# Kernel optimization log

Measured on AMD Instinct MI355X. Metric: run time of the kernel, lower is better.

## Reference

```python
import jax, jax.numpy as jnp
import numpy as np

TOP_P = 0.9
NEG_FILL = -1000000000.0


def _top_p_mask(logits):
    # probabilities over vocab
    probs = jax.nn.softmax(logits, axis=-1)
    # sort descending; keep the permutation to scatter the mask back
    order = jnp.argsort(-probs, axis=-1)                      # [B, V]
    ordered = jnp.take_along_axis(probs, order, axis=-1)      # [B, V]
    cum = jnp.cumsum(ordered, axis=-1)
    cum = cum.at[..., -1].set(0.0)
    cum = jnp.roll(cum, shift=1, axis=-1)                     # exclusive cumsum
    cmask = cum <= TOP_P                                      # [B, V] in sorted order
    # scatter back: selection[b, order[b, j]] = cmask[b, j]  <=>  gather by inverse perm
    inv = jnp.argsort(order, axis=-1)
    return jnp.take_along_axis(cmask, inv, axis=-1)


def setup_inputs() -> dict:
    key = jax.random.key(0)
    k1, k2 = jax.random.split(key)
    B, V = 256, 128000
    logits = jax.random.normal(k1, (B, V), dtype=jnp.float32)
    u = jax.random.uniform(k2, (B,), dtype=jnp.float32)
    return {"logits": logits, "u": u, "temperature": 1}


def reference(logits, u, temperature):
    t = jnp.asarray(temperature, dtype=logits.dtype)
    logits = logits / t
    sel = _top_p_mask(logits)
    masked = jnp.where(sel, logits, jnp.asarray(NEG_FILL, logits.dtype))
    probs = jax.nn.softmax(masked, axis=-1)                   # [B, V]
    # multinomial(num_samples=1) via inverse-CDF with uniform u
    cdf = jnp.cumsum(probs, axis=-1)
    token = jnp.sum(cdf < u[:, None], axis=-1)
    return jnp.minimum(token, probs.shape[-1] - 1)
```

## Files before the change

### kernel.cpp

```cpp
#include <hip/hip_runtime.h>

#define BLOCK 1024
#define NW (BLOCK / 64)
#define FPSCALE 8192.0f
#define INVSCALE 0x1p-13f

__device__ __forceinline__ float wincl(float v, int lane) {
#pragma unroll
    for (int o = 1; o < 64; o <<= 1) {
        float x = __shfl_up(v, o, 64);
        if (lane >= o) v += x;
    }
    return v;
}

__device__ __forceinline__ void find_crit_desc(const float* h, int n, int seg,
                                               float limit, int lane, int* out_b) {
    float segsum = 0.f;
    int start = n - 1 - lane * seg;
    for (int k = 0; k < seg; k++) segsum += h[start - k];
    float incl = wincl(segsum, lane);
    unsigned long long mk = __ballot(incl > limit);
    if (mk == 0ULL) { *out_b = 0; return; }
    int fl = __ffsll(mk) - 1;
    float base = __shfl(incl, fl, 64) - __shfl(segsum, fl, 64);
    int sstart = n - 1 - fl * seg;
    float v = (lane < seg) ? h[sstart - lane] : 0.f;
    float incl2 = wincl(v, lane);
    unsigned long long mk2 = __ballot((lane < seg) && (base + incl2 > limit));
    int k2 = mk2 ? (__ffsll(mk2) - 1) : (seg - 1);
    *out_b = sstart - k2;
}

#define OKEY(bb) ((bb) ^ ((unsigned)((int)(bb) >> 31) | 0x80000000u))

#define LD4(j) (*(const float4*)(row + (j)))

__global__ __launch_bounds__(BLOCK) void NucleusSampling_79336635892529_kernel(
    const float* __restrict__ logits, const float* __restrict__ uvec,
    const int* __restrict__ temp, int* __restrict__ out, int Vv) {
    const int b = blockIdx.x;
    const float* __restrict__ row = logits + (size_t)b * (size_t)Vv;
    const int t = threadIdx.x;
    const int lane = t & 63;
    const int wave = t >> 6;
    const int rep = lane & 3;

    __shared__ __align__(16) unsigned histbuf[8192];
    __shared__ float mg[2048];
    __shared__ float sweep[NW];
    __shared__ float csum[128];
    __shared__ int shb1;

    const float inv_t = 1.0f / (float)temp[0];
    const int V4 = Vv & ~3;
    const int S = BLOCK * 4;
    const int nch = (Vv + 1023) >> 10;

    for (int i = t; i < 8192; i += BLOCK) histbuf[i] = 0u;
    __syncthreads();

#define P1(xx) { unsigned kk = OKEY(__float_as_uint(xx)); \
                 float e = __expf((xx) * inv_t); \
                 atomicAdd(&histbuf[((kk >> 21) << 2) | rep], \
                           (unsigned)(e * FPSCALE + 0.5f)); }
    {
        int i = t * 4;
        bool have = (i + 3 * S + 3 < V4);
        float4 a0, a1, a2, a3;
        if (have) { a0 = LD4(i); a1 = LD4(i + S); a2 = LD4(i + 2 * S); a3 = LD4(i + 3 * S); }
        while (have) {
            const int ni = i + 4 * S;
            const bool nhave = (ni + 3 * S + 3 < V4);
            float4 n0, n1, n2, n3;
            if (nhave) { n0 = LD4(ni); n1 = LD4(ni + S); n2 = LD4(ni + 2 * S); n3 = LD4(ni + 3 * S); }
            P1(a0.x); P1(a0.y); P1(a0.z); P1(a0.w);
            P1(a1.x); P1(a1.y); P1(a1.z); P1(a1.w);
            P1(a2.x); P1(a2.y); P1(a2.z); P1(a2.w);
            P1(a3.x); P1(a3.y); P1(a3.z); P1(a3.w);
            a0 = n0; a1 = n1; a2 = n2; a3 = n3;
            i = ni; have = nhave;
        }
        for (; i < V4; i += S) { float4 a = LD4(i); P1(a.x); P1(a.y); P1(a.z); P1(a.w); }
        for (int j = V4 + t; j < Vv; j += BLOCK) P1(row[j]);
    }
    __syncthreads();

    float zp = 0.f;
    for (int i = t; i < 2048; i += BLOCK) {
        uint4 m4 = *(const uint4*)&histbuf[i << 2];
        float m = (float)(m4.x + m4.y + m4.z + m4.w) * INVSCALE;
        mg[i] = m;
        zp += m;
    }
#pragma unroll
    for (int o = 32; o >= 1; o >>= 1) zp += __shfl_xor(zp, o, 64);
    if (lane == 0) sweep[wave] = zp;
    __syncthreads();
    float Z = 0.f;
    for (int w = 0; w < NW; w++) Z += sweep[w];
    const float limit = 0.9f * Z;

    if (wave == 0) {
        int b1w;
        find_crit_desc(mg, 2048, 32, limit, lane, &b1w);
        if (lane == 0) shb1 = b1w;
    }
    if (t < 128 && t >= nch) csum[t] = 0.f;
    __syncthreads();
    const unsigned Tlow = (unsigned)shb1 << 21;

#define P2(xx, ss) { unsigned kk = OKEY(__float_as_uint(xx)); \
                     float e = __expf((xx) * inv_t); \
                     if (kk >= Tlow) ss += e; }
    for (int c0 = wave; c0 < nch; c0 += 4 * NW) {
        int cc0 = c0, cc1 = c0 + NW, cc2 = c0 + 2 * NW, cc3 = c0 + 3 * NW;
        float4 buf[4][4];
        bool val[4], full[4];
        int cbase[4] = {cc0 << 10, cc1 << 10, cc2 << 10, cc3 << 10};
        int cidx[4] = {cc0, cc1, cc2, cc3};
#pragma unroll
        for (int q = 0; q < 4; q++) {
            val[q] = (cidx[q] < nch);
            full[q] = val[q] && (cbase[q] + 1024 <= Vv);
            if (full[q]) {
                buf[q][0] = LD4(cbase[q] + lane * 4);
                buf[q][1] = LD4(cbase[q] + 256 + lane * 4);
                buf[q][2] = LD4(cbase[q] + 512 + lane * 4);
                buf[q][3] = LD4(cbase[q] + 768 + lane * 4);
            }
        }
#pragma unroll
        for (int q = 0; q < 4; q++) {
            if (!val[q]) continue;
            float s = 0.f;
            if (full[q]) {
#pragma unroll
                for (int r = 0; r < 4; r++) {
                    P2(buf[q][r].x, s); P2(buf[q][r].y, s);
                    P2(buf[q][r].z, s); P2(buf[q][r].w, s);
                }
            } else {
                for (int qq = 0; qq < 16; qq++) {
                    int i = cbase[q] + (qq << 6) + lane;
                    if (i < Vv) { float x = row[i]; P2(x, s); }
                }
            }
#pragma unroll
            for (int o = 32; o >= 1; o >>= 1) s += __shfl_xor(s, o, 64);
            if (lane == 0) csum[cidx[q]] = s;
        }
    }
    __syncthreads();

    if (wave == 0) {
        float segsum = csum[lane * 2] + csum[lane * 2 + 1];
        float incl = wincl(segsum, lane);
        float total = __shfl(incl, 63, 64);
        const float U = uvec[b] * total;
        unsigned long long mk = __ballot(incl >= U);
        int token;
        if (mk == 0ULL) {
            token = Vv;
        } else {
            int fl = __ffsll(mk) - 1;
            float base = __shfl(incl, fl, 64) - __shfl(segsum, fl, 64);
            float v = (lane < 2) ? csum[fl * 2 + lane] : 0.f;
            float incl2 = wincl(v, lane);
            unsigned long long mk2 = __ballot((lane < 2) && (base + incl2 >= U));
            int k2i = mk2 ? (__ffsll(mk2) - 1) : 1;
            int cx = fl * 2 + k2i;
            float B = base + __shfl(incl2, k2i, 64) - __shfl(v, k2i, 64);
            int cb = cx << 10;
            float vv[16];
#pragma unroll
            for (int r = 0; r < 16; r++) {
                int idx = cb + r * 64 + lane;
                vv[r] = (idx < Vv) ? row[idx] : -1e30f;
            }
            int cnt2 = 0;
#pragma unroll
            for (int r = 0; r < 16; r++) {
                int idx = cb + r * 64 + lane;
                unsigned kk = OKEY(__float_as_uint(vv[r]));
                float e = __expf(vv[r] * inv_t);
                float keep = (kk >= Tlow) ? e : 0.f;
                float is = wincl(keep, lane);
                unsigned long long mm = __ballot((idx < Vv) && (B + is < U));
                cnt2 += __popcll(mm);
                B += __shfl(is, 63, 64);
            }
            token = cb + cnt2;
        }
        if (lane == 0) out[b] = (token < Vv - 1) ? token : (Vv - 1);
    }
}

extern "C" void kernel_launch(void* const* d_in, const int* in_sizes, int n_in,
                              void* d_out, int out_size, void* d_ws, size_t ws_size,
                              hipStream_t stream) {
    const float* logits = (const float*)d_in[0];
    const float* u = (const float*)d_in[1];
    const int* temp = (const int*)d_in[2];
    int* out = (int*)d_out;
    int B = in_sizes[1];
    int V = in_sizes[0] / B;
    NucleusSampling_79336635892529_kernel<<<B, BLOCK, 0, stream>>>(logits, u, temp, out, V);
}
```

Measured before the change: 210.9 us.

## Keep half of each wave's row slice in registers between histogram and sum passes

Each wave now owns a contiguous block of eight 1024-element chunks. The first four chunks are loaded into registers and kept across the threshold-finding step, so the second pass reuses them instead of reloading from global or L2 memory. The remaining four chunks are still reloaded in pairs. This cuts second-pass memory traffic roughly in half at the cost of 64 extra live VGPRs per thread with 1024-thread blocks. It also assumes each wave covers 8192 elements, which only spans the whole row when V is at most 131072.

```diff
diff --git a/kernel.cpp b/kernel.cpp
--- a/kernel.cpp
+++ b/kernel.cpp
@@ -36,6 +36,15 @@
 
 #define LD4(j) (*(const float4*)(row + (j)))
 
+#define P1(xx) { unsigned kk = OKEY(__float_as_uint(xx)); \
+                 float e = __expf((xx) * inv_t); \
+                 atomicAdd(&histbuf[((kk >> 21) << 2) | rep], \
+                           (unsigned)(e * FPSCALE + 0.5f)); }
+
+#define P2(xx, ss) { unsigned kk = OKEY(__float_as_uint(xx)); \
+                     float e = __expf((xx) * inv_t); \
+                     if (kk >= Tlow) ss += e; }
+
 __global__ __launch_bounds__(BLOCK) void NucleusSampling_79336635892529_kernel(
     const float* __restrict__ logits, const float* __restrict__ uvec,
     const int* __restrict__ temp, int* __restrict__ out, int Vv) {
@@ -53,36 +62,70 @@
     __shared__ int shb1;
 
     const float inv_t = 1.0f / (float)temp[0];
-    const int V4 = Vv & ~3;
-    const int S = BLOCK * 4;
     const int nch = (Vv + 1023) >> 10;
 
     for (int i = t; i < 8192; i += BLOCK) histbuf[i] = 0u;
-    __syncthreads();
-
-#define P1(xx) { unsigned kk = OKEY(__float_as_uint(xx)); \
-                 float e = __expf((xx) * inv_t); \
-                 atomicAdd(&histbuf[((kk >> 21) << 2) | rep], \
-                           (unsigned)(e * FPSCALE + 0.5f)); }
-    {
-        int i = t * 4;
-        bool have = (i + 3 * S + 3 < V4);
-        float4 a0, a1, a2, a3;
-        if (have) { a0 = LD4(i); a1 = LD4(i + S); a2 = LD4(i + 2 * S); a3 = LD4(i + 3 * S); }
-        while (have) {
-            const int ni = i + 4 * S;
-            const bool nhave = (ni + 3 * S + 3 < V4);
-            float4 n0, n1, n2, n3;
-            if (nhave) { n0 = LD4(ni); n1 = LD4(ni + S); n2 = LD4(ni + 2 * S); n3 = LD4(ni + 3 * S); }
-            P1(a0.x); P1(a0.y); P1(a0.z); P1(a0.w);
-            P1(a1.x); P1(a1.y); P1(a1.z); P1(a1.w);
-            P1(a2.x); P1(a2.y); P1(a2.z); P1(a2.w);
-            P1(a3.x); P1(a3.y); P1(a3.z); P1(a3.w);
-            a0 = n0; a1 = n1; a2 = n2; a3 = n3;
-            i = ni; have = nhave;
-        }
-        for (; i < V4; i += S) { float4 a = LD4(i); P1(a.x); P1(a.y); P1(a.z); P1(a.w); }
-        for (int j = V4 + t; j < Vv; j += BLOCK) P1(row[j]);
+    if (t < 128) csum[t] = 0.f;
+    __syncthreads();
+
+    const int base0 = wave << 13;
+    float4 r[4][4];
+
+#pragma unroll
+    for (int c = 0; c < 4; c++) {
+        const int bA = base0 + (c << 10);
+        if (bA + 1024 <= Vv) {
+#pragma unroll
+            for (int q = 0; q < 4; q++) r[c][q] = LD4(bA + (q << 8) + (lane << 2));
+        }
+    }
+#pragma unroll
+    for (int c = 0; c < 4; c++) {
+        const int bA = base0 + (c << 10);
+        if (bA + 1024 <= Vv) {
+#pragma unroll
+            for (int q = 0; q < 4; q++) {
+                P1(r[c][q].x); P1(r[c][q].y); P1(r[c][q].z); P1(r[c][q].w);
+            }
+        } else if (bA < Vv) {
+            for (int qq = 0; qq < 16; qq++) {
+                int i = bA + (qq << 6) + lane;
+                if (i < Vv) P1(row[i]);
+            }
+        }
+    }
+#pragma unroll
+    for (int p = 0; p < 2; p++) {
+        const int bA = base0 + ((4 + 2 * p) << 10);
+        const int bB = bA + 1024;
+        const bool fa = (bA + 1024 <= Vv), fb = (bB + 1024 <= Vv);
+        float4 ta[4], tb[4];
+        if (fa) {
+#pragma unroll
+            for (int q = 0; q < 4; q++) ta[q] = LD4(bA + (q << 8) + (lane << 2));
+        }
+        if (fb) {
+#pragma unroll
+            for (int q = 0; q < 4; q++) tb[q] = LD4(bB + (q << 8) + (lane << 2));
+        }
+        if (fa) {
+#pragma unroll
+            for (int q = 0; q < 4; q++) { P1(ta[q].x); P1(ta[q].y); P1(ta[q].z); P1(ta[q].w); }
+        } else if (bA < Vv) {
+            for (int qq = 0; qq < 16; qq++) {
+                int i = bA + (qq << 6) + lane;
+                if (i < Vv) P1(row[i]);
+            }
+        }
+        if (fb) {
+#pragma unroll
+            for (int q = 0; q < 4; q++) { P1(tb[q].x); P1(tb[q].y); P1(tb[q].z); P1(tb[q].w); }
+        } else if (bB < Vv) {
+            for (int qq = 0; qq < 16; qq++) {
+                int i = bB + (qq << 6) + lane;
+                if (i < Vv) P1(row[i]);
+            }
+        }
     }
     __syncthreads();
 
@@ -106,49 +149,86 @@
         find_crit_desc(mg, 2048, 32, limit, lane, &b1w);
         if (lane == 0) shb1 = b1w;
     }
-    if (t < 128 && t >= nch) csum[t] = 0.f;
     __syncthreads();
     const unsigned Tlow = (unsigned)shb1 << 21;
 
-#define P2(xx, ss) { unsigned kk = OKEY(__float_as_uint(xx)); \
-                     float e = __expf((xx) * inv_t); \
-                     if (kk >= Tlow) ss += e; }
-    for (int c0 = wave; c0 < nch; c0 += 4 * NW) {
-        int cc0 = c0, cc1 = c0 + NW, cc2 = c0 + 2 * NW, cc3 = c0 + 3 * NW;
-        float4 buf[4][4];
-        bool val[4], full[4];
-        int cbase[4] = {cc0 << 10, cc1 << 10, cc2 << 10, cc3 << 10};
-        int cidx[4] = {cc0, cc1, cc2, cc3};
-#pragma unroll
-        for (int q = 0; q < 4; q++) {
-            val[q] = (cidx[q] < nch);
-            full[q] = val[q] && (cbase[q] + 1024 <= Vv);
-            if (full[q]) {
-                buf[q][0] = LD4(cbase[q] + lane * 4);
-                buf[q][1] = LD4(cbase[q] + 256 + lane * 4);
-                buf[q][2] = LD4(cbase[q] + 512 + lane * 4);
-                buf[q][3] = LD4(cbase[q] + 768 + lane * 4);
-            }
-        }
-#pragma unroll
-        for (int q = 0; q < 4; q++) {
-            if (!val[q]) continue;
-            float s = 0.f;
-            if (full[q]) {
-#pragma unroll
-                for (int r = 0; r < 4; r++) {
-                    P2(buf[q][r].x, s); P2(buf[q][r].y, s);
-                    P2(buf[q][r].z, s); P2(buf[q][r].w, s);
-                }
-            } else {
-                for (int qq = 0; qq < 16; qq++) {
-                    int i = cbase[q] + (qq << 6) + lane;
-                    if (i < Vv) { float x = row[i]; P2(x, s); }
-                }
-            }
-#pragma unroll
-            for (int o = 32; o >= 1; o >>= 1) s += __shfl_xor(s, o, 64);
-            if (lane == 0) csum[cidx[q]] = s;
+#pragma unroll
+    for (int c = 0; c < 4; c++) {
+        const int cc = (wave << 3) + c;
+        const int bA = base0 + (c << 10);
+        if (bA + 1024 <= Vv) {
+            float s = 0.f;
+#pragma unroll
+            for (int q = 0; q < 4; q++) {
+                P2(r[c][q].x, s); P2(r[c][q].y, s); P2(r[c][q].z, s); P2(r[c][q].w, s);
+            }
+#pragma unroll
+            for (int o = 32; o >= 1; o >>= 1) s += __shfl_xor(s, o, 64);
+            if (lane == 0) csum[cc] = s;
+        } else if (bA < Vv) {
+            float s = 0.f;
+            for (int qq = 0; qq < 16; qq++) {
+                int i = bA + (qq << 6) + lane;
+                if (i < Vv) { float x = row[i]; P2(x, s); }
+            }
+#pragma unroll
+            for (int o = 32; o >= 1; o >>= 1) s += __shfl_xor(s, o, 64);
+            if (lane == 0) csum[cc] = s;
+        }
+    }
+#pragma unroll
+    for (int p = 0; p < 2; p++) {
+        const int ccA = (wave << 3) + 4 + 2 * p;
+        const int ccB = ccA + 1;
+        const int bA = base0 + ((4 + 2 * p) << 10);
+        const int bB = bA + 1024;
+        const bool fa = (bA + 1024 <= Vv), fb = (bB + 1024 <= Vv);
+        float4 ta[4], tb[4];
+        if (fa) {
+#pragma unroll
+            for (int q = 0; q < 4; q++) ta[q] = LD4(bA + (q << 8) + (lane << 2));
+        }
+        if (fb) {
+#pragma unroll
+            for (int q = 0; q < 4; q++) tb[q] = LD4(bB + (q << 8) + (lane << 2));
+        }
+        if (fa) {
+            float s = 0.f;
+#pragma unroll
+            for (int q = 0; q < 4; q++) {
+                P2(ta[q].x, s); P2(ta[q].y, s); P2(ta[q].z, s); P2(ta[q].w, s);
+            }
+#pragma unroll
+            for (int o = 32; o >= 1; o >>= 1) s += __shfl_xor(s, o, 64);
+            if (lane == 0) csum[ccA] = s;
+        } else if (bA < Vv) {
+            float s = 0.f;
+            for (int qq = 0; qq < 16; qq++) {
+                int i = bA + (qq << 6) + lane;
+                if (i < Vv) { float x = row[i]; P2(x, s); }
+            }
+#pragma unroll
+            for (int o = 32; o >= 1; o >>= 1) s += __shfl_xor(s, o, 64);
+            if (lane == 0) csum[ccA] = s;
+        }
+        if (fb) {
+            float s = 0.f;
+#pragma unroll
+            for (int q = 0; q < 4; q++) {
+                P2(tb[q].x, s); P2(tb[q].y, s); P2(tb[q].z, s); P2(tb[q].w, s);
+            }
+#pragma unroll
+            for (int o = 32; o >= 1; o >>= 1) s += __shfl_xor(s, o, 64);
+            if (lane == 0) csum[ccB] = s;
+        } else if (bB < Vv) {
+            float s = 0.f;
+            for (int qq = 0; qq < 16; qq++) {
+                int i = bB + (qq << 6) + lane;
+                if (i < Vv) { float x = row[i]; P2(x, s); }
+            }
+#pragma unroll
+            for (int o = 32; o >= 1; o >>= 1) s += __shfl_xor(s, o, 64);
+            if (lane == 0) csum[ccB] = s;
         }
     }
     __syncthreads();
@@ -174,16 +254,16 @@
             int cb = cx << 10;
             float vv[16];
 #pragma unroll
-            for (int r = 0; r < 16; r++) {
-                int idx = cb + r * 64 + lane;
-                vv[r] = (idx < Vv) ? row[idx] : -1e30f;
+            for (int rr = 0; rr < 16; rr++) {
+                int idx = cb + rr * 64 + lane;
+                vv[rr] = (idx < Vv) ? row[idx] : -1e30f;
             }
             int cnt2 = 0;
 #pragma unroll
-            for (int r = 0; r < 16; r++) {
-                int idx = cb + r * 64 + lane;
-                unsigned kk = OKEY(__float_as_uint(vv[r]));
-                float e = __expf(vv[r] * inv_t);
+            for (int rr = 0; rr < 16; rr++) {
+                int idx = cb + rr * 64 + lane;
+                unsigned kk = OKEY(__float_as_uint(vv[rr]));
+                float e = __expf(vv[rr] * inv_t);
                 float keep = (kk >= Tlow) ? e : 0.f;
                 float is = wincl(keep, lane);
                 unsigned long long mm = __ballot((idx < Vv) && (B + is < U));
```

Result: faster. 205.5 us (-2.6%).
